# Performance work log

Hardware: AMD Instinct MI355X
Metric: run time of the kernel (lower is better)

Reference implementation:

```python
import jax, jax.numpy as jnp
from jax import lax
import numpy as np

GEO, CH, K, PAD = 3, 32, 5, 2


def conv(x, w, b, pad):
    y = lax.conv_general_dilated(x, w, (1, 1), [(pad, pad), (pad, pad)],
                                 dimension_numbers=('NCHW', 'OIHW', 'NCHW'))
    return y + b[None, :, None, None]


def bn(x, g, be, m, v):
    # inference-mode BatchNorm2d with running stats, eps=1e-5
    scale = g / jnp.sqrt(v + 1e-5)
    return (x - m[None, :, None, None]) * scale[None, :, None, None] + be[None, :, None, None]


def deform_conv(x, offsets, w, b, k, pad):
    # x: [B,C,H,W], offsets: [B,2*k*k,H,W] laid out as (dy,dx) per kernel tap
    B, C, H, W = x.shape
    kk = k * k
    off = offsets.reshape(B, kk, 2, H, W)
    ky, kx = jnp.meshgrid(jnp.arange(k), jnp.arange(k), indexing='ij')
    ky = ky.reshape(kk).astype(x.dtype)
    kx = kx.reshape(kk).astype(x.dtype)
    base_y = (jnp.arange(H, dtype=x.dtype) - pad)[None, None, :, None]
    base_x = (jnp.arange(W, dtype=x.dtype) - pad)[None, None, None, :]
    py = base_y + ky[None, :, None, None] + off[:, :, 0]  # [B,kk,H,W]
    px = base_x + kx[None, :, None, None] + off[:, :, 1]
    y0 = jnp.floor(py)
    x0 = jnp.floor(px)
    wy = py - y0
    wx = px - x0
    y0i = y0.astype(jnp.int32)
    x0i = x0.astype(jnp.int32)

    def corner(yi, xi):
        valid = ((yi >= 0) & (yi < H) & (xi >= 0) & (xi < W)).astype(x.dtype)
        yc = jnp.clip(yi, 0, H - 1)
        xc = jnp.clip(xi, 0, W - 1)
        # per-batch gather: [C,H,W] indexed by [kk,H,W] -> [C,kk,H,W]
        g = jax.vmap(lambda xb, yy, xx: xb[:, yy, xx])(x, yc, xc)
        return g * valid[:, None]

    v = (corner(y0i, x0i) * ((1 - wy) * (1 - wx))[:, None]
         + corner(y0i, x0i + 1) * ((1 - wy) * wx)[:, None]
         + corner(y0i + 1, x0i) * (wy * (1 - wx))[:, None]
         + corner(y0i + 1, x0i + 1) * (wy * wx)[:, None])  # [B,C,kk,H,W]
    out = jnp.einsum('bckhw,ock->bohw', v, w.reshape(w.shape[0], C, kk))
    return out + b[None, :, None, None]


def setup_inputs() -> dict:
    key = jax.random.key(0)
    ks = list(jax.random.split(key, 32))

    def wc(k, o, i, s, scale=1.0):
        return jax.random.normal(k, (o, i, s, s), jnp.float32) * (scale / np.sqrt(i * s * s))

    def vec(k, n, scale=0.1):
        return jax.random.normal(k, (n,), jnp.float32) * scale

    d = {}
    d['recon_geo'] = jax.random.normal(ks[0], (4, 4, GEO, 160, 160), jnp.float32)
    d['w1'] = wc(ks[1], CH, GEO, 5); d['b1'] = vec(ks[2], CH)
    d['g1'] = 1.0 + vec(ks[3], CH); d['be1'] = vec(ks[4], CH)
    d['m1'] = vec(ks[5], CH); d['v1'] = 0.5 + jax.random.uniform(ks[6], (CH,), jnp.float32)
    d['w2'] = wc(ks[7], CH, CH, 5); d['b2'] = vec(ks[8], CH)
    d['g2'] = 1.0 + vec(ks[9], CH); d['be2'] = vec(ks[10], CH)
    d['m2'] = vec(ks[11], CH); d['v2'] = 0.5 + jax.random.uniform(ks[12], (CH,), jnp.float32)
    d['w3'] = wc(ks[13], CH, CH, 3); d['b3'] = vec(ks[14], CH)
    d['wo'] = wc(ks[15], 2 * K * K, CH, 5, scale=0.1); d['bo'] = vec(ks[16], 2 * K * K, scale=0.0)
    d['wd'] = wc(ks[17], CH, CH, 5); d['bd'] = vec(ks[18], CH)
    d['w4'] = wc(ks[19], CH, CH, 3); d['b4'] = vec(ks[20], CH)
    d['g4'] = 1.0 + vec(ks[21], CH); d['be4'] = vec(ks[22], CH)
    d['m4'] = vec(ks[23], CH); d['v4'] = 0.5 + jax.random.uniform(ks[24], (CH,), jnp.float32)
    d['w5'] = wc(ks[25], GEO, CH, 3); d['b5'] = vec(ks[26], GEO)
    return d


def reference(recon_geo, w1, b1, g1, be1, m1, v1, w2, b2, g2, be2, m2, v2,
              w3, b3, wo, bo, wd, bd, w4, b4, g4, be4, m4, v4, w5, b5):
    B, N, C, H, W = recon_geo.shape
    x = recon_geo.reshape(B * N, C, H, W)
    # each_model
    x = jax.nn.relu(bn(conv(x, w1, b1, 2), g1, be1, m1, v1))
    x = jax.nn.relu(bn(conv(x, w2, b2, 2), g2, be2, m2, v2))
    x = conv(x, w3, b3, 1)
    x = x.reshape(B, N, CH, H, W).mean(axis=1)
    # deformable conv: learned per-pixel offsets, then bilinear-gather conv
    offsets = conv(x, wo, bo, PAD)
    x = deform_conv(x, offsets, wd, bd, K, PAD)
    # all_model
    x = jax.nn.relu(bn(conv(x, w4, b4, 1), g4, be4, m4, v4))
    x = conv(x, w5, b5, 1)
    return jnp.tanh(x[:, None])  # [B,1,GEO,H,W]
```

## Files before the change

### kernel.cpp

```cpp
#include <hip/hip_runtime.h>
#include <hip/hip_bf16.h>

#define DI static __device__ __forceinline__

typedef __attribute__((ext_vector_type(8)))  short short8v;
typedef __attribute__((ext_vector_type(4)))  short short4v;
typedef __attribute__((ext_vector_type(4)))  float float4v;
typedef __attribute__((ext_vector_type(16))) float f32x16;

namespace {
constexpr int H = 160, W = 160, HW = H * W;

constexpr int Q1 = 0;
constexpr int Q2 = 12800;
constexpr int Q3 = 38400;
constexpr int QO = 47616;
constexpr int Q4 = 98816;
constexpr int Q5 = 108032;
constexpr int QD = 117248;
constexpr int QEND = 142848;

constexpr size_t FPB = 285696;
constexpr int B1 = 0, B2 = 32, B3 = 64, BO = 96, BD = 160, B4 = 192, B5 = 224;
constexpr int NFP = 256;

constexpr size_t ACTB = 286720;
constexpr size_t A1 = 0;
constexpr size_t A2 = 13107200;
constexpr size_t AM = 26214400;
constexpr size_t AO = 29491200;
constexpr size_t AD = 36044800;
constexpr size_t A4 = 39321600;

constexpr int NPREP = QEND + 256;
}

DI float b2f(short s) {
    unsigned int u = ((unsigned int)(unsigned short)s) << 16;
    float f; __builtin_memcpy(&f, &u, 4); return f;
}
DI short f2b(float f) {
    __hip_bfloat16 h = __float2bfloat16(f);
    short s; __builtin_memcpy(&s, &h, 2); return s;
}

DI void fragw(int j, const float* __restrict__ w, const float* g, const float* v,
              int IC, int KS, int ICS, int NT, int OC, short* __restrict__ dst) {
    int q = j & 7;
    int l = (j >> 3) & 63;
    int rest = j >> 9;
    int nt = rest % NT, s = rest / NT;
    int h = s % ICS, tap = s / ICS;
    int oc = nt * 32 + (l & 31);
    int ic = h * 16 + (l >> 5) * 8 + q;
    float val = 0.f;
    if (oc < OC && ic < IC) {
        val = w[((size_t)(oc * IC + ic)) * (KS * KS) + tap];
        if (g) val *= g[oc] * rsqrtf(v[oc] + 1e-5f);
    }
    dst[j] = f2b(val);
}

__global__ void prep_k(
    const float* __restrict__ w1, const float* __restrict__ b1, const float* __restrict__ g1,
    const float* __restrict__ be1, const float* __restrict__ m1, const float* __restrict__ v1,
    const float* __restrict__ w2, const float* __restrict__ b2, const float* __restrict__ g2,
    const float* __restrict__ be2, const float* __restrict__ m2, const float* __restrict__ v2,
    const float* __restrict__ w3, const float* __restrict__ b3,
    const float* __restrict__ wo, const float* __restrict__ bo,
    const float* __restrict__ wd, const float* __restrict__ bd,
    const float* __restrict__ w4, const float* __restrict__ b4, const float* __restrict__ g4,
    const float* __restrict__ be4, const float* __restrict__ m4, const float* __restrict__ v4,
    const float* __restrict__ w5, const float* __restrict__ b5,
    short* __restrict__ q, float* __restrict__ fp)
{
    int j = blockIdx.x * 256 + threadIdx.x;
    if (j >= NPREP) return;
    if (j < Q2)   { fragw(j - Q1, w1, g1, v1, 3, 5, 1, 1, 32, q + Q1); return; }
    if (j < Q3)   { fragw(j - Q2, w2, g2, v2, 32, 5, 2, 1, 32, q + Q2); return; }
    if (j < QO)   { fragw(j - Q3, w3, nullptr, nullptr, 32, 3, 2, 1, 32, q + Q3); return; }
    if (j < Q4)   { fragw(j - QO, wo, nullptr, nullptr, 32, 5, 2, 2, 50, q + QO); return; }
    if (j < Q5)   { fragw(j - Q4, w4, g4, v4, 32, 3, 2, 1, 32, q + Q4); return; }
    if (j < QD)   { fragw(j - Q5, w5, nullptr, nullptr, 32, 3, 2, 1, 3, q + Q5); return; }
    if (j < QEND) { fragw(j - QD, wd, nullptr, nullptr, 32, 5, 2, 1, 32, q + QD); return; }
    j -= QEND;
    if (j < 32) { float s = g1[j] * rsqrtf(v1[j] + 1e-5f); fp[B1 + j] = s * (b1[j] - m1[j]) + be1[j]; return; } j -= 32;
    if (j < 32) { float s = g2[j] * rsqrtf(v2[j] + 1e-5f); fp[B2 + j] = s * (b2[j] - m2[j]) + be2[j]; return; } j -= 32;
    if (j < 32) { fp[B3 + j] = b3[j]; return; } j -= 32;
    if (j < 64) { fp[BO + j] = (j < 50) ? bo[j] : 0.f; return; } j -= 64;
    if (j < 32) { fp[BD + j] = bd[j]; return; } j -= 32;
    if (j < 32) { float s = g4[j] * rsqrtf(v4[j] + 1e-5f); fp[B4 + j] = s * (b4[j] - m4[j]) + be4[j]; return; } j -= 32;
    if (j < 32) { fp[B5 + j] = (j < 3) ? b5[j] : 0.f; return; }
}

template<int KS, int ICS, int NT, int NACC, int OMODE, bool RELU, bool IN3>
__global__ __launch_bounds__(256) void mconv_k(
    const void* __restrict__ inv, const short* __restrict__ wq,
    const float* __restrict__ bias, void* __restrict__ outv)
{
    constexpr int PAD = KS / 2, RR = 3 + KS, XX = 31 + KS;
    constexpr int PB = IN3 ? 40 : 72;
    constexpr int NS = KS * KS * ICS;
    __shared__ __align__(16) char lds[RR * XX * PB];

    const int tid = threadIdx.x, w = tid >> 6, l = tid & 63, lx = l & 31, lh = l >> 5;
    const int b = blockIdx.x;
    const int xt = b % 5, yt = (b / 5) % 40, og = b / 200;
    const int gx0 = xt * 32 - PAD, gy0 = yt * 4 - PAD;

    f32x16 acc[NT];
#pragma unroll
    for (int nt = 0; nt < NT; ++nt)
#pragma unroll
        for (int i = 0; i < 16; ++i) acc[nt][i] = 0.f;

    for (int n = 0; n < NACC; ++n) {
        if (n) __syncthreads();
        const int img = og * NACC + n;
        if (IN3) {
            const float* inb = (const float*)inv + (size_t)img * 3 * HW;
            for (int p = tid; p < RR * XX; p += 256) {
                int yy = p / XX, xx = p % XX, gy = gy0 + yy, gx = gx0 + xx;
                bool ok = (gy >= 0) & (gy < H) & (gx >= 0) & (gx < W);
                size_t o = (size_t)gy * W + gx;
                short4v v; v[0] = ok ? f2b(inb[o]) : (short)0;
                v[1] = ok ? f2b(inb[HW + o]) : (short)0;
                v[2] = ok ? f2b(inb[2 * HW + o]) : (short)0; v[3] = 0;
                short4v z; z[0] = z[1] = z[2] = z[3] = 0;
                char* dst = lds + p * PB;
                *(short4v*)dst = v;
                *(short4v*)(dst + 8) = z;
                *(short4v*)(dst + 16) = z;
                *(short4v*)(dst + 24) = z;
            }
        } else {
            const short* inb = (const short*)inv + (size_t)img * HW * 32;
            for (int c = tid; c < RR * XX * 8; c += 256) {
                int p = c >> 3, cc = c & 7;
                int yy = p / XX, xx = p % XX, gy = gy0 + yy, gx = gx0 + xx;
                short4v v;
                if ((gy >= 0) & (gy < H) & (gx >= 0) & (gx < W))
                    v = *(const short4v*)(inb + ((size_t)gy * W + gx) * 32 + cc * 4);
                else { v[0] = v[1] = v[2] = v[3] = 0; }
                *(short4v*)(lds + p * PB + cc * 8) = v;
            }
        }
        __syncthreads();

#pragma unroll
        for (int s = 0; s < NS; ++s) {
            const int tap = s / ICS, hh = s % ICS;
            const int ky = tap / KS, kx = tap % KS;
            const char* ap = lds + ((w + ky) * XX + lx + kx) * PB + hh * 32 + lh * 16;
            union { short4v h[2]; short8v v; } u;
            u.h[0] = *(const short4v*)ap;
            u.h[1] = *(const short4v*)(ap + 8);
#pragma unroll
            for (int nt = 0; nt < NT; ++nt) {
                short8v bf = *(const short8v*)(wq + ((size_t)(s * NT + nt) * 64 + l) * 8);
                acc[nt] = __builtin_amdgcn_mfma_f32_32x32x16_bf16(u.v, bf, acc[nt], 0, 0, 0);
            }
        }
    }

    constexpr float MS = (NACC == 4) ? 0.25f : 1.f;
    const int y = yt * 4 + w;
    if (OMODE == 0) {
        const float bb = bias[lx];
        short* ob = (short*)outv + ((size_t)og * HW + (size_t)y * W + xt * 32) * 32 + lx;
#pragma unroll
        for (int r = 0; r < 16; ++r) {
            int row = (r & 3) + 8 * (r >> 2) + 4 * lh;
            float vv = acc[0][r] * MS + bb;
            if (RELU) vv = fmaxf(vv, 0.f);
            ob[(size_t)row * 32] = f2b(vv);
        }
    } else if (OMODE == 1) {
        short* ob = (short*)outv + ((size_t)og * HW + (size_t)y * W + xt * 32) * 64;
#pragma unroll
        for (int nt = 0; nt < NT; ++nt) {
            const int oc = nt * 32 + lx;
            const float bb = bias[oc];
#pragma unroll
            for (int r = 0; r < 16; ++r) {
                int row = (r & 3) + 8 * (r >> 2) + 4 * lh;
                ob[(size_t)row * 64 + oc] = f2b(acc[nt][r] + bb);
            }
        }
    } else {
        const int oc = lx;
        const float bb = bias[oc];
        float* ob = (float*)outv;
#pragma unroll
        for (int r = 0; r < 16; ++r) {
            int row = (r & 3) + 8 * (r >> 2) + 4 * lh;
            float vv = tanhf(acc[0][r] + bb);
            if (oc < 3)
                ob[(((size_t)og * 3 + oc) * H + y) * W + xt * 32 + row] = vv;
        }
    }
}

__global__ __launch_bounds__(256) void deform_m_k(
    const short* __restrict__ xn,
    const short* __restrict__ offs,
    const short* __restrict__ wq,
    const float* __restrict__ bias,
    short* __restrict__ out)
{
    __shared__ float red[3][64][16];

    const int tid = threadIdx.x, w = tid >> 6, l = tid & 63, lx = l & 31, lh = l >> 5;
    const int S = blockIdx.x;
    const int x0 = (S % 5) * 32;
    const int y  = (S / 5) % H;
    const int img = S / 800;
    const int px = x0 + lx;

    const short* xb = xn + (size_t)img * HW * 32;
    const short* op = offs + ((size_t)img * HW + (size_t)y * W + px) * 64;

    f32x16 acc;
#pragma unroll
    for (int i = 0; i < 16; ++i) acc[i] = 0.f;

    for (int t = w; t < 25; t += 4) {
        const int ky = t / 5, kx = t % 5;
        unsigned int oo = *(const unsigned int*)(op + 2 * t);
        float dy = b2f((short)(oo & 0xffff));
        float dx = b2f((short)(oo >> 16));
        float py  = (float)(y - 2 + ky) + dy;
        float pxf = (float)(px - 2 + kx) + dx;
        float fy = floorf(py), fx = floorf(pxf);
        float wy = py - fy, wx = pxf - fx;
        int iy = (int)fy, ix = (int)fx;

        float wgt[4]; const short* cp[4]; bool ok[4];
#pragma unroll
        for (int c = 0; c < 4; ++c) {
            int yy = iy + (c >> 1), xx = ix + (c & 1);
            ok[c] = (yy >= 0) & (yy < H) & (xx >= 0) & (xx < W);
            wgt[c] = ((c >> 1) ? wy : 1.f - wy) * ((c & 1) ? wx : 1.f - wx);
            cp[c] = xb + ((size_t)yy * W + xx) * 32;
        }

#pragma unroll
        for (int h = 0; h < 2; ++h) {
            const int ic0 = h * 16 + lh * 8;
            float va[8];
#pragma unroll
            for (int j = 0; j < 8; ++j) va[j] = 0.f;
#pragma unroll
            for (int c = 0; c < 4; ++c) {
                if (ok[c]) {
                    short8v g = *(const short8v*)(cp[c] + ic0);
#pragma unroll
                    for (int j = 0; j < 8; ++j) va[j] = fmaf(wgt[c], b2f(g[j]), va[j]);
                }
            }
            short8v u;
#pragma unroll
            for (int j = 0; j < 8; ++j) u[j] = f2b(va[j]);
            short8v bf = *(const short8v*)(wq + ((size_t)(t * 2 + h) * 64 + l) * 8);
            acc = __builtin_amdgcn_mfma_f32_32x32x16_bf16(u, bf, acc, 0, 0, 0);
        }
    }

    if (w) {
        float* rp = &red[w - 1][l][0];
#pragma unroll
        for (int r4 = 0; r4 < 4; ++r4) {
            float4v v; v[0] = acc[r4 * 4]; v[1] = acc[r4 * 4 + 1];
            v[2] = acc[r4 * 4 + 2]; v[3] = acc[r4 * 4 + 3];
            *(float4v*)(rp + r4 * 4) = v;
        }
    }
    __syncthreads();
    if (w == 0) {
#pragma unroll
        for (int j = 0; j < 3; ++j) {
            const float* rp = &red[j][l][0];
#pragma unroll
            for (int r4 = 0; r4 < 4; ++r4) {
                float4v v = *(const float4v*)(rp + r4 * 4);
                acc[r4 * 4] += v[0]; acc[r4 * 4 + 1] += v[1];
                acc[r4 * 4 + 2] += v[2]; acc[r4 * 4 + 3] += v[3];
            }
        }
        const float bb = bias[lx];
        short* ob = out + ((size_t)img * HW + (size_t)y * W + x0) * 32 + lx;
#pragma unroll
        for (int r = 0; r < 16; ++r) {
            int row = (r & 3) + 8 * (r >> 2) + 4 * lh;
            ob[(size_t)row * 32] = f2b(acc[r] + bb);
        }
    }
}

extern "C" void kernel_launch(void* const* d_in, const int* in_sizes, int n_in,
                              void* d_out, int out_size, void* d_ws, size_t ws_size,
                              hipStream_t stream)
{
    const float* rg  = (const float*)d_in[0];
    const float* w1  = (const float*)d_in[1];  const float* b1 = (const float*)d_in[2];
    const float* g1  = (const float*)d_in[3];  const float* be1 = (const float*)d_in[4];
    const float* m1  = (const float*)d_in[5];  const float* v1 = (const float*)d_in[6];
    const float* w2  = (const float*)d_in[7];  const float* b2 = (const float*)d_in[8];
    const float* g2  = (const float*)d_in[9];  const float* be2 = (const float*)d_in[10];
    const float* m2  = (const float*)d_in[11]; const float* v2 = (const float*)d_in[12];
    const float* w3  = (const float*)d_in[13]; const float* b3 = (const float*)d_in[14];
    const float* wo  = (const float*)d_in[15]; const float* bo = (const float*)d_in[16];
    const float* wd  = (const float*)d_in[17]; const float* bd = (const float*)d_in[18];
    const float* w4  = (const float*)d_in[19]; const float* b4 = (const float*)d_in[20];
    const float* g4  = (const float*)d_in[21]; const float* be4 = (const float*)d_in[22];
    const float* m4  = (const float*)d_in[23]; const float* v4 = (const float*)d_in[24];
    const float* w5  = (const float*)d_in[25]; const float* b5 = (const float*)d_in[26];

    short* q   = (short*)d_ws;
    float* fp  = (float*)((char*)d_ws + FPB);
    short* act = (short*)((char*)d_ws + ACTB);
    short* act1  = act + A1;
    short* act2  = act + A2;
    short* amean = act + AM;
    short* aoffs = act + AO;
    short* adf   = act + AD;
    short* a4o   = act + A4;

    prep_k<<<NPREP / 256, 256, 0, stream>>>(
        w1, b1, g1, be1, m1, v1, w2, b2, g2, be2, m2, v2, w3, b3,
        wo, bo, wd, bd, w4, b4, g4, be4, m4, v4, w5, b5, q, fp);

    mconv_k<5, 1, 1, 1, 0, true,  true ><<<3200, 256, 0, stream>>>(rg,   q + Q1, fp + B1, act1);
    mconv_k<5, 2, 1, 1, 0, true,  false><<<3200, 256, 0, stream>>>(act1, q + Q2, fp + B2, act2);
    mconv_k<3, 2, 1, 4, 0, false, false><<< 800, 256, 0, stream>>>(act2, q + Q3, fp + B3, amean);

    mconv_k<5, 2, 2, 1, 1, false, false><<< 800, 256, 0, stream>>>(amean, q + QO, fp + BO, aoffs);
    deform_m_k<<<3200, 256, 0, stream>>>(amean, aoffs, q + QD, fp + BD, adf);
    mconv_k<3, 2, 1, 1, 0, true,  false><<< 800, 256, 0, stream>>>(adf,  q + Q4, fp + B4, a4o);
    mconv_k<3, 2, 1, 1, 2, false, false><<< 800, 256, 0, stream>>>(a4o,  q + Q5, fp + B5, d_out);
}
```

Before: 278.0 us.

## Permute offset channels per wave and restructure LDS reduction layout

The offset conv output channels are permuted so that each wave's seven taps (t = w, w+4, ...) are stored contiguously, letting each wave fetch all of its offsets with two 16-byte loads up front instead of a scattered 4-byte load per tap. The tap loop is fully unrolled with a guard for t<25. The cross-wave reduction buffer in LDS is changed to a strided scalar layout, replacing float4 accesses. This touches both the producer (offset conv epilogue) and the consumer (deform kernel), and assumes the permutation is applied to every consumer of the offset buffer.

```diff
diff --git a/kernel.cpp b/kernel.cpp
--- a/kernel.cpp
+++ b/kernel.cpp
@@ -42,6 +42,18 @@
 DI short f2b(float f) {
     __hip_bfloat16 h = __float2bfloat16(f);
     short s; __builtin_memcpy(&s, &h, 2); return s;
+}
+
+DI int offs_perm(int oc) {
+    if (oc < 50) {
+        int t = oc >> 1, d = oc & 1;
+        return (t & 3) * 16 + (t >> 2) * 2 + d;
+    }
+    int i = oc - 50;
+    if (i < 2)  return 14 + i;
+    if (i < 6)  return 28 + (i - 2);
+    if (i < 10) return 44 + (i - 6);
+    return 60 + (i - 10);
 }
 
 DI void fragw(int j, const float* __restrict__ w, const float* g, const float* v,
@@ -181,10 +193,11 @@
         for (int nt = 0; nt < NT; ++nt) {
             const int oc = nt * 32 + lx;
             const float bb = bias[oc];
+            const int nc = offs_perm(oc);
 #pragma unroll
             for (int r = 0; r < 16; ++r) {
                 int row = (r & 3) + 8 * (r >> 2) + 4 * lh;
-                ob[(size_t)row * 64 + oc] = f2b(acc[nt][r] + bb);
+                ob[(size_t)row * 64 + nc] = f2b(acc[nt][r] + bb);
             }
         }
     } else {
@@ -208,7 +221,7 @@
     const float* __restrict__ bias,
     short* __restrict__ out)
 {
-    __shared__ float red[3][64][16];
+    __shared__ float red[3 * 16 * 64];
 
     const int tid = threadIdx.x, w = tid >> 6, l = tid & 63, lx = l & 31, lh = l >> 5;
     const int S = blockIdx.x;
@@ -218,74 +231,73 @@
     const int px = x0 + lx;
 
     const short* xb = xn + (size_t)img * HW * 32;
-    const short* op = offs + ((size_t)img * HW + (size_t)y * W + px) * 64;
+    const short* op2 = offs + ((size_t)img * HW + (size_t)y * W + px) * 64 + w * 16;
+
+    union { short8v v2[2]; short s[16]; } pp;
+    pp.v2[0] = *(const short8v*)(op2);
+    pp.v2[1] = *(const short8v*)(op2 + 8);
 
     f32x16 acc;
 #pragma unroll
     for (int i = 0; i < 16; ++i) acc[i] = 0.f;
 
-    for (int t = w; t < 25; t += 4) {
-        const int ky = t / 5, kx = t % 5;
-        unsigned int oo = *(const unsigned int*)(op + 2 * t);
-        float dy = b2f((short)(oo & 0xffff));
-        float dx = b2f((short)(oo >> 16));
-        float py  = (float)(y - 2 + ky) + dy;
-        float pxf = (float)(px - 2 + kx) + dx;
-        float fy = floorf(py), fx = floorf(pxf);
-        float wy = py - fy, wx = pxf - fx;
-        int iy = (int)fy, ix = (int)fx;
-
-        float wgt[4]; const short* cp[4]; bool ok[4];
-#pragma unroll
-        for (int c = 0; c < 4; ++c) {
-            int yy = iy + (c >> 1), xx = ix + (c & 1);
-            ok[c] = (yy >= 0) & (yy < H) & (xx >= 0) & (xx < W);
-            wgt[c] = ((c >> 1) ? wy : 1.f - wy) * ((c & 1) ? wx : 1.f - wx);
-            cp[c] = xb + ((size_t)yy * W + xx) * 32;
-        }
-
-#pragma unroll
-        for (int h = 0; h < 2; ++h) {
-            const int ic0 = h * 16 + lh * 8;
-            float va[8];
-#pragma unroll
-            for (int j = 0; j < 8; ++j) va[j] = 0.f;
+#pragma unroll
+    for (int tt = 0; tt < 7; ++tt) {
+        const int t = 4 * tt + w;
+        if (t < 25) {
+            const int ky = t / 5, kx = t % 5;
+            float dy = b2f(pp.s[2 * tt]);
+            float dx = b2f(pp.s[2 * tt + 1]);
+            float py  = (float)(y - 2 + ky) + dy;
+            float pxf = (float)(px - 2 + kx) + dx;
+            float fy = floorf(py), fx = floorf(pxf);
+            float wy = py - fy, wx = pxf - fx;
+            int iy = (int)fy, ix = (int)fx;
+
+            float wgt[4]; const short* cp[4]; bool ok[4];
 #pragma unroll
             for (int c = 0; c < 4; ++c) {
-                if (ok[c]) {
-                    short8v g = *(const short8v*)(cp[c] + ic0);
-#pragma unroll
-                    for (int j = 0; j < 8; ++j) va[j] = fmaf(wgt[c], b2f(g[j]), va[j]);
+                int yy = iy + (c >> 1), xx = ix + (c & 1);
+                ok[c] = (yy >= 0) & (yy < H) & (xx >= 0) & (xx < W);
+                wgt[c] = ((c >> 1) ? wy : 1.f - wy) * ((c & 1) ? wx : 1.f - wx);
+                cp[c] = xb + ((size_t)yy * W + xx) * 32;
+            }
+
+#pragma unroll
+            for (int h = 0; h < 2; ++h) {
+                const int ic0 = h * 16 + lh * 8;
+                float va[8];
+#pragma unroll
+                for (int j = 0; j < 8; ++j) va[j] = 0.f;
+#pragma unroll
+                for (int c = 0; c < 4; ++c) {
+                    if (ok[c]) {
+                        short8v g = *(const short8v*)(cp[c] + ic0);
+#pragma unroll
+                        for (int j = 0; j < 8; ++j) va[j] = fmaf(wgt[c], b2f(g[j]), va[j]);
+                    }
                 }
-            }
-            short8v u;
-#pragma unroll
-            for (int j = 0; j < 8; ++j) u[j] = f2b(va[j]);
-            short8v bf = *(const short8v*)(wq + ((size_t)(t * 2 + h) * 64 + l) * 8);
-            acc = __builtin_amdgcn_mfma_f32_32x32x16_bf16(u, bf, acc, 0, 0, 0);
+                short8v u;
+#pragma unroll
+                for (int j = 0; j < 8; ++j) u[j] = f2b(va[j]);
+                short8v bf = *(const short8v*)(wq + ((size_t)(t * 2 + h) * 64 + l) * 8);
+                acc = __builtin_amdgcn_mfma_f32_32x32x16_bf16(u, bf, acc, 0, 0, 0);
+            }
         }
     }
 
     if (w) {
-        float* rp = &red[w - 1][l][0];
-#pragma unroll
-        for (int r4 = 0; r4 < 4; ++r4) {
-            float4v v; v[0] = acc[r4 * 4]; v[1] = acc[r4 * 4 + 1];
-            v[2] = acc[r4 * 4 + 2]; v[3] = acc[r4 * 4 + 3];
-            *(float4v*)(rp + r4 * 4) = v;
-        }
+        float* rp = &red[(w - 1) * 16 * 64 + l];
+#pragma unroll
+        for (int r = 0; r < 16; ++r) rp[r * 64] = acc[r];
     }
     __syncthreads();
     if (w == 0) {
 #pragma unroll
         for (int j = 0; j < 3; ++j) {
-            const float* rp = &red[j][l][0];
-#pragma unroll
-            for (int r4 = 0; r4 < 4; ++r4) {
-                float4v v = *(const float4v*)(rp + r4 * 4);
-                acc[r4 * 4] += v[0]; acc[r4 * 4 + 1] += v[1];
-                acc[r4 * 4 + 2] += v[2]; acc[r4 * 4 + 3] += v[3];
-            }
+            const float* rp = &red[j * 16 * 64 + l];
+#pragma unroll
+            for (int r = 0; r < 16; ++r) acc[r] += rp[r * 64];
         }
         const float bb = bias[lx];
         short* ob = out + ((size_t)img * HW + (size_t)y * W + x0) * 32 + lx;
```

Result: faster. 267.1 us (-3.9%).
